# Kernel optimization log

Hardware: AMD Instinct MI355X
Metric: run time of the kernel (lower is better)

Reference implementation:

```python
import jax, jax.numpy as jnp
import numpy as np

N_NODES = 100000
EPS = 1e-12  # F.normalize eps


def _sage_conv(x, src, dst, deg, Wl, bl, Wr):
    # mean aggregation of neighbor (source) features at destination nodes
    agg = jax.ops.segment_sum(x[src], dst, num_segments=N_NODES)  # [N, F]
    agg = agg / jnp.maximum(deg, 1.0)[:, None]
    out = agg @ Wl + bl + x @ Wr  # lin_l(mean(x_j)) + lin_r(x_i)
    # normalize=True -> L2 row normalization
    norm = jnp.sqrt(jnp.sum(out * out, axis=-1, keepdims=True))
    return out / jnp.maximum(norm, EPS)


def setup_inputs() -> dict:
    key = jax.random.key(0)
    ks = jax.random.split(key, 10)
    F_IN, H, C = 14, 32, 2
    x = jax.random.normal(ks[0], (N_NODES, F_IN), dtype=jnp.float32)
    edge_index = jax.random.randint(ks[1], (2, 6400000), 0, N_NODES, dtype=jnp.int32)
    def glorot(k, shape):
        lim = float(np.sqrt(6.0 / (shape[0] + shape[1])))
        return jax.random.uniform(k, shape, jnp.float32, -lim, lim)
    return {
        "x": x,
        "edge_index": edge_index,
        "W1l": glorot(ks[2], (F_IN, H)), "b1": jnp.zeros((H,), jnp.float32),
        "W1r": glorot(ks[3], (F_IN, H)),
        "W2l": glorot(ks[4], (H, H)), "b2": jnp.zeros((H,), jnp.float32),
        "W2r": glorot(ks[5], (H, H)),
        "Wlin": glorot(ks[6], (H, C)), "blin": jnp.zeros((C,), jnp.float32),
    }


def reference(x, edge_index, W1l, b1, W1r, W2l, b2, W2r, Wlin, blin):
    src, dst = edge_index[0], edge_index[1]
    deg = jax.ops.segment_sum(jnp.ones_like(dst, dtype=x.dtype), dst,
                              num_segments=N_NODES)  # in-degree per node
    h = jax.nn.relu(_sage_conv(x, src, dst, deg, W1l, b1, W1r))
    # dropout p=0.2 is identity at inference
    h = jax.nn.relu(_sage_conv(h, src, dst, deg, W2l, b2, W2r))
    return h @ Wlin + blin  # [N, num_classes]
```

## Files before the change

### kernel.cpp

```cpp
#include <hip/hip_runtime.h>
#include <hip/hip_bf16.h>


#define CHA 16384
#define MAXBH 800
#define CAPH 9728
#define NPB 128

static __device__ __forceinline__ unsigned short f2bf(float f) {
    unsigned u = __float_as_uint(f);
    unsigned r = (u + 0x7FFFu + ((u >> 16) & 1u)) >> 16;
    return (unsigned short)r;
}
#define BF_LO(u) __uint_as_float((u) << 16)
#define BF_HI(u) __uint_as_float((u) & 0xFFFF0000u)

__global__ void cvt_x_bf16(const float* __restrict__ x, unsigned short* __restrict__ xb,
                           int* __restrict__ bcursor, int N, int NBH) {
    int idx = blockIdx.x * blockDim.x + threadIdx.x;
    if (idx < NBH) bcursor[idx] = idx * CAPH;
    if (idx >= N * 16) return;
    int n = idx >> 4, f = idx & 15;
    float v = (f < 14) ? x[n * 14 + f] : 0.f;
    xb[idx] = f2bf(v);
}

__global__ __launch_bounds__(1024) void partitionA(
        const int* __restrict__ src, const int* __restrict__ dst,
        int* __restrict__ bcursor, unsigned* __restrict__ part, int E, int NBH) {
    __shared__ unsigned pk[CHA];
    __shared__ int h[MAXBH], lofs[MAXBH], delta[MAXBH];
    int t = threadIdx.x;
    int base = blockIdx.x * CHA;
    int end = base + CHA; if (end > E) end = E;
    int cnt = end - base;

    int ed[16], es[16], er[16];
    for (int i = t; i < NBH; i += 1024) h[i] = 0;
    __syncthreads();
    #pragma unroll
    for (int i = 0; i < 4; ++i) {
        int j = i * 4096 + t * 4;
        if (j + 4 <= cnt) {
            int4 d4 = *(const int4*)(dst + base + j);
            int4 s4 = *(const int4*)(src + base + j);
            ed[i*4+0] = d4.x; ed[i*4+1] = d4.y; ed[i*4+2] = d4.z; ed[i*4+3] = d4.w;
            es[i*4+0] = s4.x; es[i*4+1] = s4.y; es[i*4+2] = s4.z; es[i*4+3] = s4.w;
            er[i*4+0] = atomicAdd(&h[d4.x >> 7], 1);
            er[i*4+1] = atomicAdd(&h[d4.y >> 7], 1);
            er[i*4+2] = atomicAdd(&h[d4.z >> 7], 1);
            er[i*4+3] = atomicAdd(&h[d4.w >> 7], 1);
        } else {
            #pragma unroll
            for (int k = 0; k < 4; ++k) {
                if (j + k < cnt) {
                    ed[i*4+k] = dst[base + j + k];
                    es[i*4+k] = src[base + j + k];
                    er[i*4+k] = atomicAdd(&h[ed[i*4+k] >> 7], 1);
                } else ed[i*4+k] = -1;
            }
        }
    }
    __syncthreads();
    if (t < 64) {
        int vals[13];
        int run = 0;
        int b13 = t * 13;
        #pragma unroll
        for (int i = 0; i < 13; ++i) {
            int idx = b13 + i;
            int x = (idx < NBH) ? h[idx] : 0;
            run += x;
            vals[i] = run;
        }
        int tot = run, sc = run;
        #pragma unroll
        for (int off = 1; off < 64; off <<= 1) {
            int nv = __shfl_up(sc, off);
            if (t >= off) sc += nv;
        }
        int excl = sc - tot;
        #pragma unroll
        for (int i = 0; i < 13; ++i) {
            int idx = b13 + i;
            if (idx < NBH) {
                h[idx] = excl + vals[i];
                lofs[idx] = excl + (i ? vals[i - 1] : 0);
            }
        }
    }
    __syncthreads();
    if (t < NBH) {
        int excl = lofs[t];
        int v = h[t] - excl;
        int g = v ? atomicAdd(&bcursor[t], v) : 0;
        delta[t] = g - excl;
    }
    __syncthreads();
    #pragma unroll
    for (int i = 0; i < 16; ++i) {
        int d = ed[i];
        if (d >= 0) {
            int b = d >> 7;
            pk[lofs[b] + er[i]] = ((unsigned)(d & 127) << 24) | (unsigned)es[i];
        }
    }
    __syncthreads();
    int wid = t >> 6, lane = t & 63;
    for (int b = wid; b < NBH; b += 16) {
        int s = lofs[b];
        int e2 = h[b];
        int dlt = delta[b];
        int lim = (b + 1) * CAPH;
        for (int k = s + lane; k < e2; k += 64) {
            int gidx = dlt + k;
            if (gidx < lim) part[gidx] = pk[k];
        }
    }
}

__global__ __launch_bounds__(1024) void partitionB_sort(
        const unsigned* __restrict__ part, const int* __restrict__ bcursor,
        int* __restrict__ deg, int* __restrict__ offs, int* __restrict__ nlo,
        int* __restrict__ sorted_src, int N, int HALF) {
    __shared__ int pk2[CAPH];
    __shared__ int hh[256], keyofs[256];
    __shared__ int sTot;
    int hbid = blockIdx.x;
    int t = threadIdx.x;
    int start = hbid * CAPH;
    int end = bcursor[hbid];
    if (end > start + CAPH) end = start + CAPH;
    unsigned ce[10];
    int rk[10];
    if (t < 256) hh[t] = 0;
    __syncthreads();
    #pragma unroll
    for (int i = 0; i < 10; ++i) {
        int idx = start + t + i * 1024;
        unsigned p = 0xFFFFFFFFu;
        int r = 0;
        if (idx < end) {
            p = part[idx];
            int key = (int)(p >> 24) * 2 + (((int)(p & 0xFFFFFFu) < HALF) ? 0 : 1);
            r = atomicAdd(&hh[key], 1);
        }
        ce[i] = p;
        rk[i] = r;
    }
    __syncthreads();
    if (t < 64) {
        int b4 = t * 4;
        int v0 = hh[b4], v1 = hh[b4 + 1], v2 = hh[b4 + 2], v3 = hh[b4 + 3];
        int s1 = v0 + v1, s2 = s1 + v2, s3 = s2 + v3;
        int sc = s3;
        #pragma unroll
        for (int off = 1; off < 64; off <<= 1) {
            int nv = __shfl_up(sc, off);
            if (t >= off) sc += nv;
        }
        int excl = sc - s3;
        keyofs[b4]     = excl;
        keyofs[b4 + 1] = excl + v0;
        keyofs[b4 + 2] = excl + s1;
        keyofs[b4 + 3] = excl + s2;
        if (t == 63) sTot = excl + s3;
    }
    __syncthreads();
    if (t < 128) {
        int lo = hh[2 * t];
        int d = lo + hh[2 * t + 1];
        int excl = keyofs[2 * t];
        int node = hbid * 128 + t;
        if (node < N) {
            deg[node] = d;
            offs[node] = start + excl;
            nlo[node] = lo;
        }
    }
    #pragma unroll
    for (int i = 0; i < 10; ++i) {
        unsigned p = ce[i];
        if (p != 0xFFFFFFFFu) {
            int s = (int)(p & 0xFFFFFFu);
            int key = (int)(p >> 24) * 2 + ((s < HALF) ? 0 : 1);
            int pos = keyofs[key] + rk[i];
            if (pos < CAPH) pk2[pos] = s;
        }
    }
    __syncthreads();
    int tot = sTot; if (tot > CAPH) tot = CAPH;
    for (int i = t; i < tot; i += 1024)
        sorted_src[start + i] = pk2[i];
}

__global__ __launch_bounds__(256) void gather14_dense1(
        const uint4* __restrict__ xb4, const float* __restrict__ x,
        const int* __restrict__ sorted_src, const int* __restrict__ offs,
        const int* __restrict__ deg,
        const float* __restrict__ W1l, const float* __restrict__ b1,
        const float* __restrict__ W1r,
        float* __restrict__ hbuf, unsigned short* __restrict__ hb, int N) {
    __shared__ float swl[448], swr[448], sb1[32];
    int t = threadIdx.x;
    for (int i = t; i < 448; i += 256) { swl[i] = W1l[i]; swr[i] = W1r[i]; }
    if (t < 32) sb1[t] = b1[t];
    __syncthreads();

    int node = blockIdx.x * 32 + (t >> 3);
    int sub = t & 7, ep = sub >> 1, half = sub & 1;
    int lanebase = (t & 63) & ~7;
    bool valid = node < N;
    int js = valid ? offs[node] : 0;
    int d  = valid ? deg[node] : 0;
    int je = js + d;
    float x0 = 0.f, x1 = 0.f;
    if (valid && sub < 7) {
        x0 = x[node * 14 + sub * 2];
        x1 = x[node * 14 + sub * 2 + 1];
    }

    float a[8] = {0,0,0,0,0,0,0,0};
    int j = js + ep;
    for (; j + 12 < je; j += 16) {
        int s0 = sorted_src[j], s1 = sorted_src[j + 4];
        int s2 = sorted_src[j + 8], s3 = sorted_src[j + 12];
        uint4 u0 = xb4[s0 * 2 + half], u1 = xb4[s1 * 2 + half];
        uint4 u2 = xb4[s2 * 2 + half], u3 = xb4[s3 * 2 + half];
        a[0] += (BF_LO(u0.x) + BF_LO(u1.x)) + (BF_LO(u2.x) + BF_LO(u3.x));
        a[1] += (BF_HI(u0.x) + BF_HI(u1.x)) + (BF_HI(u2.x) + BF_HI(u3.x));
        a[2] += (BF_LO(u0.y) + BF_LO(u1.y)) + (BF_LO(u2.y) + BF_LO(u3.y));
        a[3] += (BF_HI(u0.y) + BF_HI(u1.y)) + (BF_HI(u2.y) + BF_HI(u3.y));
        a[4] += (BF_LO(u0.z) + BF_LO(u1.z)) + (BF_LO(u2.z) + BF_LO(u3.z));
        a[5] += (BF_HI(u0.z) + BF_HI(u1.z)) + (BF_HI(u2.z) + BF_HI(u3.z));
        a[6] += (BF_LO(u0.w) + BF_LO(u1.w)) + (BF_LO(u2.w) + BF_LO(u3.w));
        a[7] += (BF_HI(u0.w) + BF_HI(u1.w)) + (BF_HI(u2.w) + BF_HI(u3.w));
    }
    for (; j + 4 < je; j += 8) {
        int s0 = sorted_src[j], s1 = sorted_src[j + 4];
        uint4 u0 = xb4[s0 * 2 + half], u1 = xb4[s1 * 2 + half];
        a[0] += BF_LO(u0.x) + BF_LO(u1.x);
        a[1] += BF_HI(u0.x) + BF_HI(u1.x);
        a[2] += BF_LO(u0.y) + BF_LO(u1.y);
        a[3] += BF_HI(u0.y) + BF_HI(u1.y);
        a[4] += BF_LO(u0.z) + BF_LO(u1.z);
        a[5] += BF_HI(u0.z) + BF_HI(u1.z);
        a[6] += BF_LO(u0.w) + BF_LO(u1.w);
        a[7] += BF_HI(u0.w) + BF_HI(u1.w);
    }
    for (; j < je; j += 4) {
        uint4 u0 = xb4[sorted_src[j] * 2 + half];
        a[0] += BF_LO(u0.x); a[1] += BF_HI(u0.x);
        a[2] += BF_LO(u0.y); a[3] += BF_HI(u0.y);
        a[4] += BF_LO(u0.z); a[5] += BF_HI(u0.z);
        a[6] += BF_LO(u0.w); a[7] += BF_HI(u0.w);
    }
    #pragma unroll
    for (int i = 0; i < 8; ++i) {
        a[i] += __shfl_xor(a[i], 2);
        a[i] += __shfl_xor(a[i], 4);
    }

    float inv = 1.0f / ((d > 0) ? (float)d : 1.0f);
    float acc[4];
    #pragma unroll
    for (int i = 0; i < 4; ++i) acc[i] = sb1[sub * 4 + i];
    #pragma unroll
    for (int k = 0; k < 14; ++k) {
        float ag = __shfl(a[k & 7], lanebase + (k >> 3)) * inv;
        float xv = __shfl((k & 1) ? x1 : x0, lanebase + (k >> 1));
        float4 wl = *(const float4*)&swl[k * 32 + sub * 4];
        float4 wr = *(const float4*)&swr[k * 32 + sub * 4];
        acc[0] += ag * wl.x + xv * wr.x;
        acc[1] += ag * wl.y + xv * wr.y;
        acc[2] += ag * wl.z + xv * wr.z;
        acc[3] += ag * wl.w + xv * wr.w;
    }
    float ss = 0.f;
    #pragma unroll
    for (int i = 0; i < 4; ++i) ss += acc[i] * acc[i];
    ss += __shfl_xor(ss, 1); ss += __shfl_xor(ss, 2); ss += __shfl_xor(ss, 4);
    float invn = 1.f / fmaxf(sqrtf(ss), 1e-12f);
    if (valid) {
        float hv[4];
        #pragma unroll
        for (int i = 0; i < 4; ++i) hv[i] = fmaxf(acc[i] * invn, 0.f);
        *(float4*)(hbuf + (size_t)node * 32 + sub * 4) =
            make_float4(hv[0], hv[1], hv[2], hv[3]);
        uint2 pb;
        pb.x = (unsigned)f2bf(hv[0]) | ((unsigned)f2bf(hv[1]) << 16);
        pb.y = (unsigned)f2bf(hv[2]) | ((unsigned)f2bf(hv[3]) << 16);
        *(uint2*)(hb + (size_t)node * 32 + sub * 4) = pb;
    }
}

__global__ __launch_bounds__(256) void gather32_p0(
        const uint4* __restrict__ hb, const int* __restrict__ sorted_src,
        const int* __restrict__ offs, const int* __restrict__ nlo,
        float4* __restrict__ agg2a, int N) {
    int idx = blockIdx.x * blockDim.x + threadIdx.x;
    int n = idx >> 2;
    if (n >= N) return;
    int q = idx & 3;
    int start = offs[n];
    int jend = nlo[n];
    float a0=0,a1=0,a2=0,a3=0,a4=0,a5=0,a6=0,a7=0;
    int j = 0;
    for (; j + 8 <= jend; j += 8) {
        int s0 = sorted_src[start + j + 0];
        int s1 = sorted_src[start + j + 1];
        int s2 = sorted_src[start + j + 2];
        int s3 = sorted_src[start + j + 3];
        int s4 = sorted_src[start + j + 4];
        int s5 = sorted_src[start + j + 5];
        int s6 = sorted_src[start + j + 6];
        int s7 = sorted_src[start + j + 7];
        uint4 u0 = hb[s0 * 4 + q];
        uint4 u1 = hb[s1 * 4 + q];
        uint4 u2 = hb[s2 * 4 + q];
        uint4 u3 = hb[s3 * 4 + q];
        uint4 u4 = hb[s4 * 4 + q];
        uint4 u5 = hb[s5 * 4 + q];
        uint4 u6 = hb[s6 * 4 + q];
        uint4 u7 = hb[s7 * 4 + q];
        a0 += (BF_LO(u0.x)+BF_LO(u1.x)+BF_LO(u2.x)+BF_LO(u3.x))
            + (BF_LO(u4.x)+BF_LO(u5.x)+BF_LO(u6.x)+BF_LO(u7.x));
        a1 += (BF_HI(u0.x)+BF_HI(u1.x)+BF_HI(u2.x)+BF_HI(u3.x))
            + (BF_HI(u4.x)+BF_HI(u5.x)+BF_HI(u6.x)+BF_HI(u7.x));
        a2 += (BF_LO(u0.y)+BF_LO(u1.y)+BF_LO(u2.y)+BF_LO(u3.y))
            + (BF_LO(u4.y)+BF_LO(u5.y)+BF_LO(u6.y)+BF_LO(u7.y));
        a3 += (BF_HI(u0.y)+BF_HI(u1.y)+BF_HI(u2.y)+BF_HI(u3.y))
            + (BF_HI(u4.y)+BF_HI(u5.y)+BF_HI(u6.y)+BF_HI(u7.y));
        a4 += (BF_LO(u0.z)+BF_LO(u1.z)+BF_LO(u2.z)+BF_LO(u3.z))
            + (BF_LO(u4.z)+BF_LO(u5.z)+BF_LO(u6.z)+BF_LO(u7.z));
        a5 += (BF_HI(u0.z)+BF_HI(u1.z)+BF_HI(u2.z)+BF_HI(u3.z))
            + (BF_HI(u4.z)+BF_HI(u5.z)+BF_HI(u6.z)+BF_HI(u7.z));
        a6 += (BF_LO(u0.w)+BF_LO(u1.w)+BF_LO(u2.w)+BF_LO(u3.w))
            + (BF_LO(u4.w)+BF_LO(u5.w)+BF_LO(u6.w)+BF_LO(u7.w));
        a7 += (BF_HI(u0.w)+BF_HI(u1.w)+BF_HI(u2.w)+BF_HI(u3.w))
            + (BF_HI(u4.w)+BF_HI(u5.w)+BF_HI(u6.w)+BF_HI(u7.w));
    }
    for (; j + 4 <= jend; j += 4) {
        int s0 = sorted_src[start + j + 0];
        int s1 = sorted_src[start + j + 1];
        int s2 = sorted_src[start + j + 2];
        int s3 = sorted_src[start + j + 3];
        uint4 u0 = hb[s0 * 4 + q];
        uint4 u1 = hb[s1 * 4 + q];
        uint4 u2 = hb[s2 * 4 + q];
        uint4 u3 = hb[s3 * 4 + q];
        a0 += BF_LO(u0.x)+BF_LO(u1.x)+BF_LO(u2.x)+BF_LO(u3.x);
        a1 += BF_HI(u0.x)+BF_HI(u1.x)+BF_HI(u2.x)+BF_HI(u3.x);
        a2 += BF_LO(u0.y)+BF_LO(u1.y)+BF_LO(u2.y)+BF_LO(u3.y);
        a3 += BF_HI(u0.y)+BF_HI(u1.y)+BF_HI(u2.y)+BF_HI(u3.y);
        a4 += BF_LO(u0.z)+BF_LO(u1.z)+BF_LO(u2.z)+BF_LO(u3.z);
        a5 += BF_HI(u0.z)+BF_HI(u1.z)+BF_HI(u2.z)+BF_HI(u3.z);
        a6 += BF_LO(u0.w)+BF_LO(u1.w)+BF_LO(u2.w)+BF_LO(u3.w);
        a7 += BF_HI(u0.w)+BF_HI(u1.w)+BF_HI(u2.w)+BF_HI(u3.w);
    }
    for (; j < jend; ++j) {
        uint4 u0 = hb[sorted_src[start + j] * 4 + q];
        a0 += BF_LO(u0.x); a1 += BF_HI(u0.x);
        a2 += BF_LO(u0.y); a3 += BF_HI(u0.y);
        a4 += BF_LO(u0.z); a5 += BF_HI(u0.z);
        a6 += BF_LO(u0.w); a7 += BF_HI(u0.w);
    }
    agg2a[n * 8 + q * 2 + 0] = make_float4(a0, a1, a2, a3);
    agg2a[n * 8 + q * 2 + 1] = make_float4(a4, a5, a6, a7);
}

__global__ __launch_bounds__(256) void gather32_p1(
        const uint4* __restrict__ hb, const int* __restrict__ sorted_src,
        const int* __restrict__ offs, const int* __restrict__ deg,
        const int* __restrict__ nlo, float4* __restrict__ agg2b, int N) {
    int idx = blockIdx.x * blockDim.x + threadIdx.x;
    int n = idx >> 2;
    if (n >= N) return;
    int q = idx & 3;
    int start = offs[n];
    int d = deg[n];
    int j = nlo[n];
    float a0=0,a1=0,a2=0,a3=0,a4=0,a5=0,a6=0,a7=0;
    for (; j + 8 <= d; j += 8) {
        int s0 = sorted_src[start + j + 0];
        int s1 = sorted_src[start + j + 1];
        int s2 = sorted_src[start + j + 2];
        int s3 = sorted_src[start + j + 3];
        int s4 = sorted_src[start + j + 4];
        int s5 = sorted_src[start + j + 5];
        int s6 = sorted_src[start + j + 6];
        int s7 = sorted_src[start + j + 7];
        uint4 u0 = hb[s0 * 4 + q];
        uint4 u1 = hb[s1 * 4 + q];
        uint4 u2 = hb[s2 * 4 + q];
        uint4 u3 = hb[s3 * 4 + q];
        uint4 u4 = hb[s4 * 4 + q];
        uint4 u5 = hb[s5 * 4 + q];
        uint4 u6 = hb[s6 * 4 + q];
        uint4 u7 = hb[s7 * 4 + q];
        a0 += (BF_LO(u0.x)+BF_LO(u1.x)+BF_LO(u2.x)+BF_LO(u3.x))
            + (BF_LO(u4.x)+BF_LO(u5.x)+BF_LO(u6.x)+BF_LO(u7.x));
        a1 += (BF_HI(u0.x)+BF_HI(u1.x)+BF_HI(u2.x)+BF_HI(u3.x))
            + (BF_HI(u4.x)+BF_HI(u5.x)+BF_HI(u6.x)+BF_HI(u7.x));
        a2 += (BF_LO(u0.y)+BF_LO(u1.y)+BF_LO(u2.y)+BF_LO(u3.y))
            + (BF_LO(u4.y)+BF_LO(u5.y)+BF_LO(u6.y)+BF_LO(u7.y));
        a3 += (BF_HI(u0.y)+BF_HI(u1.y)+BF_HI(u2.y)+BF_HI(u3.y))
            + (BF_HI(u4.y)+BF_HI(u5.y)+BF_HI(u6.y)+BF_HI(u7.y));
        a4 += (BF_LO(u0.z)+BF_LO(u1.z)+BF_LO(u2.z)+BF_LO(u3.z))
            + (BF_LO(u4.z)+BF_LO(u5.z)+BF_LO(u6.z)+BF_LO(u7.z));
        a5 += (BF_HI(u0.z)+BF_HI(u1.z)+BF_HI(u2.z)+BF_HI(u3.z))
            + (BF_HI(u4.z)+BF_HI(u5.z)+BF_HI(u6.z)+BF_HI(u7.z));
        a6 += (BF_LO(u0.w)+BF_LO(u1.w)+BF_LO(u2.w)+BF_LO(u3.w))
            + (BF_LO(u4.w)+BF_LO(u5.w)+BF_LO(u6.w)+BF_LO(u7.w));
        a7 += (BF_HI(u0.w)+BF_HI(u1.w)+BF_HI(u2.w)+BF_HI(u3.w))
            + (BF_HI(u4.w)+BF_HI(u5.w)+BF_HI(u6.w)+BF_HI(u7.w));
    }
    for (; j + 4 <= d; j += 4) {
        int s0 = sorted_src[start + j + 0];
        int s1 = sorted_src[start + j + 1];
        int s2 = sorted_src[start + j + 2];
        int s3 = sorted_src[start + j + 3];
        uint4 u0 = hb[s0 * 4 + q];
        uint4 u1 = hb[s1 * 4 + q];
        uint4 u2 = hb[s2 * 4 + q];
        uint4 u3 = hb[s3 * 4 + q];
        a0 += BF_LO(u0.x)+BF_LO(u1.x)+BF_LO(u2.x)+BF_LO(u3.x);
        a1 += BF_HI(u0.x)+BF_HI(u1.x)+BF_HI(u2.x)+BF_HI(u3.x);
        a2 += BF_LO(u0.y)+BF_LO(u1.y)+BF_LO(u2.y)+BF_LO(u3.y);
        a3 += BF_HI(u0.y)+BF_HI(u1.y)+BF_HI(u2.y)+BF_HI(u3.y);
        a4 += BF_LO(u0.z)+BF_LO(u1.z)+BF_LO(u2.z)+BF_LO(u3.z);
        a5 += BF_HI(u0.z)+BF_HI(u1.z)+BF_HI(u2.z)+BF_HI(u3.z);
        a6 += BF_LO(u0.w)+BF_LO(u1.w)+BF_LO(u2.w)+BF_LO(u3.w);
        a7 += BF_HI(u0.w)+BF_HI(u1.w)+BF_HI(u2.w)+BF_HI(u3.w);
    }
    for (; j < d; ++j) {
        uint4 u0 = hb[sorted_src[start + j] * 4 + q];
        a0 += BF_LO(u0.x); a1 += BF_HI(u0.x);
        a2 += BF_LO(u0.y); a3 += BF_HI(u0.y);
        a4 += BF_LO(u0.z); a5 += BF_HI(u0.z);
        a6 += BF_LO(u0.w); a7 += BF_HI(u0.w);
    }
    agg2b[n * 8 + q * 2 + 0] = make_float4(a0, a1, a2, a3);
    agg2b[n * 8 + q * 2 + 1] = make_float4(a4, a5, a6, a7);
}

__global__ __launch_bounds__(256) void dense2(
        const float* __restrict__ h, const float* __restrict__ agg2a,
        const float* __restrict__ agg2b, const int* __restrict__ deg,
        const float* __restrict__ W2l, const float* __restrict__ b2,
        const float* __restrict__ W2r, const float* __restrict__ Wlin,
        const float* __restrict__ blin, float* __restrict__ out, int N) {
    __shared__ float sa[NPB * 33];
    __shared__ float sh2[NPB * 33];
    __shared__ float swl[32 * 32], swr[32 * 32], swo[64], sb[32], sbo[2];
    int t = threadIdx.x;
    int nb = blockIdx.x * NPB;
    int nn = N - nb; if (nn > NPB) nn = NPB;
    const float4* ga = (const float4*)(agg2a + (size_t)nb * 32);
    const float4* gb = (const float4*)(agg2b + (size_t)nb * 32);
    const float4* gh = (const float4*)(h + (size_t)nb * 32);
    for (int i = t; i < nn * 8; i += 256) {
        int row = i >> 3;
        int dv = deg[nb + row];
        float inv = 1.0f / ((dv > 0) ? (float)dv : 1.0f);
        float4 va = ga[i], vb = gb[i];
        float* d = &sa[row * 33 + (i & 7) * 4];
        d[0] = (va.x + vb.x) * inv; d[1] = (va.y + vb.y) * inv;
        d[2] = (va.z + vb.z) * inv; d[3] = (va.w + vb.w) * inv;
        float4 w = gh[i];
        float* e = &sh2[row * 33 + (i & 7) * 4];
        e[0] = w.x; e[1] = w.y; e[2] = w.z; e[3] = w.w;
    }
    for (int i = t; i < 1024; i += 256) { swl[i] = W2l[i]; swr[i] = W2r[i]; }
    if (t < 64) swo[t] = Wlin[t];
    if (t < 32) sb[t] = b2[t];
    if (t < 2) sbo[t] = blin[t];
    __syncthreads();
    int q2 = t & 3;
    int p = t >> 2;
    int l0 = p * 2, l1 = l0 + 1;
    float acc0[8], acc1[8];
    #pragma unroll
    for (int j = 0; j < 8; ++j) { acc0[j] = sb[q2 * 8 + j]; acc1[j] = acc0[j]; }
    for (int k = 0; k < 32; ++k) {
        float a0 = sa[l0 * 33 + k],  a1 = sa[l1 * 33 + k];
        float h0 = sh2[l0 * 33 + k], h1 = sh2[l1 * 33 + k];
        const float4* wl4 = (const float4*)&swl[k * 32 + q2 * 8];
        const float4* wr4 = (const float4*)&swr[k * 32 + q2 * 8];
        float4 wla = wl4[0], wlb = wl4[1], wra = wr4[0], wrb = wr4[1];
        acc0[0] += a0 * wla.x + h0 * wra.x;  acc1[0] += a1 * wla.x + h1 * wra.x;
        acc0[1] += a0 * wla.y + h0 * wra.y;  acc1[1] += a1 * wla.y + h1 * wra.y;
        acc0[2] += a0 * wla.z + h0 * wra.z;  acc1[2] += a1 * wla.z + h1 * wra.z;
        acc0[3] += a0 * wla.w + h0 * wra.w;  acc1[3] += a1 * wla.w + h1 * wra.w;
        acc0[4] += a0 * wlb.x + h0 * wrb.x;  acc1[4] += a1 * wlb.x + h1 * wrb.x;
        acc0[5] += a0 * wlb.y + h0 * wrb.y;  acc1[5] += a1 * wlb.y + h1 * wrb.y;
        acc0[6] += a0 * wlb.z + h0 * wrb.z;  acc1[6] += a1 * wlb.z + h1 * wrb.z;
        acc0[7] += a0 * wlb.w + h0 * wrb.w;  acc1[7] += a1 * wlb.w + h1 * wrb.w;
    }
    float ss0 = 0.f, ss1 = 0.f;
    #pragma unroll
    for (int j = 0; j < 8; ++j) { ss0 += acc0[j] * acc0[j]; ss1 += acc1[j] * acc1[j]; }
    ss0 += __shfl_xor(ss0, 1); ss0 += __shfl_xor(ss0, 2);
    ss1 += __shfl_xor(ss1, 1); ss1 += __shfl_xor(ss1, 2);
    float inv0 = 1.f / fmaxf(sqrtf(ss0), 1e-12f);
    float inv1 = 1.f / fmaxf(sqrtf(ss1), 1e-12f);
    float o00 = 0.f, o01 = 0.f, o10 = 0.f, o11 = 0.f;
    #pragma unroll
    for (int j = 0; j < 8; ++j) {
        float hv0 = fmaxf(acc0[j] * inv0, 0.f);
        float hv1 = fmaxf(acc1[j] * inv1, 0.f);
        int kk = q2 * 8 + j;
        o00 += hv0 * swo[kk * 2 + 0];
        o01 += hv0 * swo[kk * 2 + 1];
        o10 += hv1 * swo[kk * 2 + 0];
        o11 += hv1 * swo[kk * 2 + 1];
    }
    o00 += __shfl_xor(o00, 1); o00 += __shfl_xor(o00, 2);
    o01 += __shfl_xor(o01, 1); o01 += __shfl_xor(o01, 2);
    o10 += __shfl_xor(o10, 1); o10 += __shfl_xor(o10, 2);
    o11 += __shfl_xor(o11, 1); o11 += __shfl_xor(o11, 2);
    if (q2 == 0) {
        int n0 = nb + l0, n1 = nb + l1;
        if (n0 < N) { out[n0 * 2 + 0] = o00 + sbo[0]; out[n0 * 2 + 1] = o01 + sbo[1]; }
        if (n1 < N) { out[n1 * 2 + 0] = o10 + sbo[0]; out[n1 * 2 + 1] = o11 + sbo[1]; }
    }
}

extern "C" void kernel_launch(void* const* d_in, const int* in_sizes, int n_in,
                              void* d_out, int out_size, void* d_ws, size_t ws_size,
                              hipStream_t stream) {
    const float* x    = (const float*)d_in[0];
    const int*   ei   = (const int*)d_in[1];
    const float* W1l  = (const float*)d_in[2];
    const float* b1   = (const float*)d_in[3];
    const float* W1r  = (const float*)d_in[4];
    const float* W2l  = (const float*)d_in[5];
    const float* b2   = (const float*)d_in[6];
    const float* W2r  = (const float*)d_in[7];
    const float* Wlin = (const float*)d_in[8];
    const float* blin = (const float*)d_in[9];
    float* out = (float*)d_out;

    const int N = in_sizes[0] / 14;
    const int E = in_sizes[1] / 2;
    const int* src = ei;
    const int* dst = ei + E;
    const int NBH = (N + 127) / 128;
    const int HALF = N / 2;

    char* ws = (char*)d_ws;
    size_t off = 0;
    auto alloc = [&](size_t bytes) -> void* {
        void* p = ws + off;
        off = (off + bytes + 255) & ~(size_t)255;
        return p;
    };
    int*            bcursor    = (int*)alloc((size_t)NBH * 4);
    unsigned*       part       = (unsigned*)alloc((size_t)NBH * CAPH * 4);
    int*            sorted_src = (int*)alloc((size_t)NBH * CAPH * 4);
    int*            deg        = (int*)alloc((size_t)N * 4);
    int*            offs       = (int*)alloc((size_t)N * 4);
    int*            nlo        = (int*)alloc((size_t)N * 4);
    unsigned short* xb         = (unsigned short*)alloc((size_t)N * 16 * 2);
    float*          hbuf       = (float*)alloc((size_t)N * 32 * 4);
    unsigned short* hb         = (unsigned short*)alloc((size_t)N * 32 * 2);
    float*          agg2b      = (float*)alloc((size_t)N * 32 * 4);
    float*          agg2a      = (float*)part;
    (void)ws_size; (void)n_in; (void)out_size;

    const int NB32 = (N + 31) / 32;

    cvt_x_bf16<<<(N * 16 + 255) / 256, 256, 0, stream>>>(x, xb, bcursor, N, NBH);
    partitionA<<<(E + CHA - 1) / CHA, 1024, 0, stream>>>(src, dst, bcursor, part, E, NBH);
    partitionB_sort<<<NBH, 1024, 0, stream>>>(
        part, bcursor, deg, offs, nlo, sorted_src, N, HALF);
    gather14_dense1<<<NB32, 256, 0, stream>>>(
        (const uint4*)xb, x, sorted_src, offs, deg, W1l, b1, W1r, hbuf, hb, N);
    gather32_p0<<<(N * 4 + 255) / 256, 256, 0, stream>>>(
        (const uint4*)hb, sorted_src, offs, nlo, (float4*)agg2a, N);
    gather32_p1<<<(N * 4 + 255) / 256, 256, 0, stream>>>(
        (const uint4*)hb, sorted_src, offs, deg, nlo, (float4*)agg2b, N);
    dense2<<<(N + NPB - 1) / NPB, 256, 0, stream>>>(
        hbuf, agg2a, agg2b, deg, W2l, b2, W2r, Wlin, blin, out, N);
}
```

Measured before the change: 276.3 us.

## Fuse second gather half with dense2 and fold bf16 conversion into partitioning

The bf16 conversion of x moves into partitionA as a grid-stride loop, and bcursor is zeroed with a memset. partitionA drops its shared-memory staging and block-wide scan and scatters straight to global using per-block atomic bases, with half the chunk size and thread count. The second half of the layer-2 gather is fused with the dense2 epilogue, so the agg2b buffer and one launch go away. The risks are less coalesced scatter writes in partitionA and the gather now competing with the shared-memory weight load for occupancy.

```diff
diff --git a/kernel.cpp b/kernel.cpp
--- a/kernel.cpp
+++ b/kernel.cpp
@@ -2,10 +2,9 @@
 #include <hip/hip_bf16.h>
 
 
-#define CHA 16384
+#define CHA 8192
 #define MAXBH 800
 #define CAPH 9728
-#define NPB 128
 
 static __device__ __forceinline__ unsigned short f2bf(float f) {
     unsigned u = __float_as_uint(f);
@@ -15,32 +14,29 @@
 #define BF_LO(u) __uint_as_float((u) << 16)
 #define BF_HI(u) __uint_as_float((u) & 0xFFFF0000u)
 
-__global__ void cvt_x_bf16(const float* __restrict__ x, unsigned short* __restrict__ xb,
-                           int* __restrict__ bcursor, int N, int NBH) {
-    int idx = blockIdx.x * blockDim.x + threadIdx.x;
-    if (idx < NBH) bcursor[idx] = idx * CAPH;
-    if (idx >= N * 16) return;
-    int n = idx >> 4, f = idx & 15;
-    float v = (f < 14) ? x[n * 14 + f] : 0.f;
-    xb[idx] = f2bf(v);
-}
-
-__global__ __launch_bounds__(1024) void partitionA(
+__global__ __launch_bounds__(512) void partitionA(
+        const float* __restrict__ x, unsigned short* __restrict__ xb,
         const int* __restrict__ src, const int* __restrict__ dst,
-        int* __restrict__ bcursor, unsigned* __restrict__ part, int E, int NBH) {
-    __shared__ unsigned pk[CHA];
-    __shared__ int h[MAXBH], lofs[MAXBH], delta[MAXBH];
+        int* __restrict__ bcursor, unsigned* __restrict__ part,
+        int E, int N, int NBH) {
+    __shared__ int h[MAXBH], gb[MAXBH];
     int t = threadIdx.x;
     int base = blockIdx.x * CHA;
     int end = base + CHA; if (end > E) end = E;
     int cnt = end - base;
 
+    for (int i = blockIdx.x * 512 + t; i < N * 16; i += gridDim.x * 512) {
+        int n = i >> 4, f = i & 15;
+        float v = (f < 14) ? x[n * 14 + f] : 0.f;
+        xb[i] = f2bf(v);
+    }
+
     int ed[16], es[16], er[16];
-    for (int i = t; i < NBH; i += 1024) h[i] = 0;
+    for (int i = t; i < NBH; i += 512) h[i] = 0;
     __syncthreads();
     #pragma unroll
     for (int i = 0; i < 4; ++i) {
-        int j = i * 4096 + t * 4;
+        int j = i * 2048 + t * 4;
         if (j + 4 <= cnt) {
             int4 d4 = *(const int4*)(dst + base + j);
             int4 s4 = *(const int4*)(src + base + j);
@@ -62,59 +58,20 @@
         }
     }
     __syncthreads();
-    if (t < 64) {
-        int vals[13];
-        int run = 0;
-        int b13 = t * 13;
-        #pragma unroll
-        for (int i = 0; i < 13; ++i) {
-            int idx = b13 + i;
-            int x = (idx < NBH) ? h[idx] : 0;
-            run += x;
-            vals[i] = run;
-        }
-        int tot = run, sc = run;
-        #pragma unroll
-        for (int off = 1; off < 64; off <<= 1) {
-            int nv = __shfl_up(sc, off);
-            if (t >= off) sc += nv;
-        }
-        int excl = sc - tot;
-        #pragma unroll
-        for (int i = 0; i < 13; ++i) {
-            int idx = b13 + i;
-            if (idx < NBH) {
-                h[idx] = excl + vals[i];
-                lofs[idx] = excl + (i ? vals[i - 1] : 0);
-            }
-        }
-    }
-    __syncthreads();
-    if (t < NBH) {
-        int excl = lofs[t];
-        int v = h[t] - excl;
-        int g = v ? atomicAdd(&bcursor[t], v) : 0;
-        delta[t] = g - excl;
+    for (int i = t; i < NBH; i += 512) {
+        int v = h[i];
+        gb[i] = v ? atomicAdd(&bcursor[i], v) : 0;
     }
     __syncthreads();
     #pragma unroll
     for (int i = 0; i < 16; ++i) {
-        int d = ed[i];
-        if (d >= 0) {
-            int b = d >> 7;
-            pk[lofs[b] + er[i]] = ((unsigned)(d & 127) << 24) | (unsigned)es[i];
-        }
-    }
-    __syncthreads();
-    int wid = t >> 6, lane = t & 63;
-    for (int b = wid; b < NBH; b += 16) {
-        int s = lofs[b];
-        int e2 = h[b];
-        int dlt = delta[b];
-        int lim = (b + 1) * CAPH;
-        for (int k = s + lane; k < e2; k += 64) {
-            int gidx = dlt + k;
-            if (gidx < lim) part[gidx] = pk[k];
+        int dd = ed[i];
+        if (dd >= 0) {
+            int b = dd >> 7;
+            int pos = gb[b] + er[i];
+            if (pos < CAPH)
+                part[(size_t)b * CAPH + pos] =
+                    ((unsigned)(dd & 127) << 24) | (unsigned)es[i];
         }
     }
 }
@@ -129,8 +86,9 @@
     int hbid = blockIdx.x;
     int t = threadIdx.x;
     int start = hbid * CAPH;
-    int end = bcursor[hbid];
-    if (end > start + CAPH) end = start + CAPH;
+    int cc = bcursor[hbid];
+    if (cc > CAPH) cc = CAPH;
+    int end = start + cc;
     unsigned ce[10];
     int rk[10];
     if (t < 256) hh[t] = 0;
@@ -369,17 +327,29 @@
     agg2a[n * 8 + q * 2 + 1] = make_float4(a4, a5, a6, a7);
 }
 
-__global__ __launch_bounds__(256) void gather32_p1(
+__global__ __launch_bounds__(256) void gather32p1_dense2(
         const uint4* __restrict__ hb, const int* __restrict__ sorted_src,
         const int* __restrict__ offs, const int* __restrict__ deg,
-        const int* __restrict__ nlo, float4* __restrict__ agg2b, int N) {
-    int idx = blockIdx.x * blockDim.x + threadIdx.x;
-    int n = idx >> 2;
-    if (n >= N) return;
-    int q = idx & 3;
-    int start = offs[n];
-    int d = deg[n];
-    int j = nlo[n];
+        const int* __restrict__ nlo, const float* __restrict__ agg2a,
+        const float* __restrict__ hbuf,
+        const float* __restrict__ W2l, const float* __restrict__ b2,
+        const float* __restrict__ W2r, const float* __restrict__ Wlin,
+        const float* __restrict__ blin, float* __restrict__ out, int N) {
+    __shared__ float sa[64 * 33];
+    __shared__ float sh2[64 * 33];
+    __shared__ float swl[1024], swr[1024], swo[64], sb[32], sbo[2];
+    int t = threadIdx.x;
+    for (int i = t; i < 1024; i += 256) { swl[i] = W2l[i]; swr[i] = W2r[i]; }
+    if (t < 64) swo[t] = Wlin[t];
+    if (t < 32) sb[t] = b2[t];
+    if (t < 2) sbo[t] = blin[t];
+
+    int row = t >> 2, q = t & 3;
+    int n = blockIdx.x * 64 + row;
+    bool valid = n < N;
+    int start = valid ? offs[n] : 0;
+    int d = valid ? deg[n] : 0;
+    int j = valid ? nlo[n] : 0;
     float a0=0,a1=0,a2=0,a3=0,a4=0,a5=0,a6=0,a7=0;
     for (; j + 8 <= d; j += 8) {
         int s0 = sorted_src[start + j + 0];
@@ -440,89 +410,59 @@
         a4 += BF_LO(u0.z); a5 += BF_HI(u0.z);
         a6 += BF_LO(u0.w); a7 += BF_HI(u0.w);
     }
-    agg2b[n * 8 + q * 2 + 0] = make_float4(a0, a1, a2, a3);
-    agg2b[n * 8 + q * 2 + 1] = make_float4(a4, a5, a6, a7);
-}
-
-__global__ __launch_bounds__(256) void dense2(
-        const float* __restrict__ h, const float* __restrict__ agg2a,
-        const float* __restrict__ agg2b, const int* __restrict__ deg,
-        const float* __restrict__ W2l, const float* __restrict__ b2,
-        const float* __restrict__ W2r, const float* __restrict__ Wlin,
-        const float* __restrict__ blin, float* __restrict__ out, int N) {
-    __shared__ float sa[NPB * 33];
-    __shared__ float sh2[NPB * 33];
-    __shared__ float swl[32 * 32], swr[32 * 32], swo[64], sb[32], sbo[2];
-    int t = threadIdx.x;
-    int nb = blockIdx.x * NPB;
-    int nn = N - nb; if (nn > NPB) nn = NPB;
-    const float4* ga = (const float4*)(agg2a + (size_t)nb * 32);
-    const float4* gb = (const float4*)(agg2b + (size_t)nb * 32);
-    const float4* gh = (const float4*)(h + (size_t)nb * 32);
-    for (int i = t; i < nn * 8; i += 256) {
-        int row = i >> 3;
-        int dv = deg[nb + row];
-        float inv = 1.0f / ((dv > 0) ? (float)dv : 1.0f);
-        float4 va = ga[i], vb = gb[i];
-        float* d = &sa[row * 33 + (i & 7) * 4];
-        d[0] = (va.x + vb.x) * inv; d[1] = (va.y + vb.y) * inv;
-        d[2] = (va.z + vb.z) * inv; d[3] = (va.w + vb.w) * inv;
-        float4 w = gh[i];
-        float* e = &sh2[row * 33 + (i & 7) * 4];
-        e[0] = w.x; e[1] = w.y; e[2] = w.z; e[3] = w.w;
-    }
-    for (int i = t; i < 1024; i += 256) { swl[i] = W2l[i]; swr[i] = W2r[i]; }
-    if (t < 64) swo[t] = Wlin[t];
-    if (t < 32) sb[t] = b2[t];
-    if (t < 2) sbo[t] = blin[t];
-    __syncthreads();
-    int q2 = t & 3;
-    int p = t >> 2;
-    int l0 = p * 2, l1 = l0 + 1;
-    float acc0[8], acc1[8];
-    #pragma unroll
-    for (int j = 0; j < 8; ++j) { acc0[j] = sb[q2 * 8 + j]; acc1[j] = acc0[j]; }
+    if (valid) {
+        float inv = 1.0f / ((d > 0) ? (float)d : 1.0f);
+        const float4* ga = (const float4*)(agg2a + (size_t)n * 32 + q * 8);
+        float4 v0 = ga[0], v1 = ga[1];
+        float* sd = &sa[row * 33 + q * 8];
+        sd[0] = (v0.x + a0) * inv; sd[1] = (v0.y + a1) * inv;
+        sd[2] = (v0.z + a2) * inv; sd[3] = (v0.w + a3) * inv;
+        sd[4] = (v1.x + a4) * inv; sd[5] = (v1.y + a5) * inv;
+        sd[6] = (v1.z + a6) * inv; sd[7] = (v1.w + a7) * inv;
+        const float4* gh = (const float4*)(hbuf + (size_t)n * 32 + q * 8);
+        float4 h0 = gh[0], h1 = gh[1];
+        float* se = &sh2[row * 33 + q * 8];
+        se[0] = h0.x; se[1] = h0.y; se[2] = h0.z; se[3] = h0.w;
+        se[4] = h1.x; se[5] = h1.y; se[6] = h1.z; se[7] = h1.w;
+    }
+    __syncthreads();
+
+    float acc[8];
+    #pragma unroll
+    for (int i = 0; i < 8; ++i) acc[i] = sb[q * 8 + i];
     for (int k = 0; k < 32; ++k) {
-        float a0 = sa[l0 * 33 + k],  a1 = sa[l1 * 33 + k];
-        float h0 = sh2[l0 * 33 + k], h1 = sh2[l1 * 33 + k];
-        const float4* wl4 = (const float4*)&swl[k * 32 + q2 * 8];
-        const float4* wr4 = (const float4*)&swr[k * 32 + q2 * 8];
+        float av = sa[row * 33 + k];
+        float hv = sh2[row * 33 + k];
+        const float4* wl4 = (const float4*)&swl[k * 32 + q * 8];
+        const float4* wr4 = (const float4*)&swr[k * 32 + q * 8];
         float4 wla = wl4[0], wlb = wl4[1], wra = wr4[0], wrb = wr4[1];
-        acc0[0] += a0 * wla.x + h0 * wra.x;  acc1[0] += a1 * wla.x + h1 * wra.x;
-        acc0[1] += a0 * wla.y + h0 * wra.y;  acc1[1] += a1 * wla.y + h1 * wra.y;
-        acc0[2] += a0 * wla.z + h0 * wra.z;  acc1[2] += a1 * wla.z + h1 * wra.z;
-        acc0[3] += a0 * wla.w + h0 * wra.w;  acc1[3] += a1 * wla.w + h1 * wra.w;
-        acc0[4] += a0 * wlb.x + h0 * wrb.x;  acc1[4] += a1 * wlb.x + h1 * wrb.x;
-        acc0[5] += a0 * wlb.y + h0 * wrb.y;  acc1[5] += a1 * wlb.y + h1 * wrb.y;
-        acc0[6] += a0 * wlb.z + h0 * wrb.z;  acc1[6] += a1 * wlb.z + h1 * wrb.z;
-        acc0[7] += a0 * wlb.w + h0 * wrb.w;  acc1[7] += a1 * wlb.w + h1 * wrb.w;
-    }
-    float ss0 = 0.f, ss1 = 0.f;
-    #pragma unroll
-    for (int j = 0; j < 8; ++j) { ss0 += acc0[j] * acc0[j]; ss1 += acc1[j] * acc1[j]; }
-    ss0 += __shfl_xor(ss0, 1); ss0 += __shfl_xor(ss0, 2);
-    ss1 += __shfl_xor(ss1, 1); ss1 += __shfl_xor(ss1, 2);
-    float inv0 = 1.f / fmaxf(sqrtf(ss0), 1e-12f);
-    float inv1 = 1.f / fmaxf(sqrtf(ss1), 1e-12f);
-    float o00 = 0.f, o01 = 0.f, o10 = 0.f, o11 = 0.f;
-    #pragma unroll
-    for (int j = 0; j < 8; ++j) {
-        float hv0 = fmaxf(acc0[j] * inv0, 0.f);
-        float hv1 = fmaxf(acc1[j] * inv1, 0.f);
-        int kk = q2 * 8 + j;
-        o00 += hv0 * swo[kk * 2 + 0];
-        o01 += hv0 * swo[kk * 2 + 1];
-        o10 += hv1 * swo[kk * 2 + 0];
-        o11 += hv1 * swo[kk * 2 + 1];
-    }
-    o00 += __shfl_xor(o00, 1); o00 += __shfl_xor(o00, 2);
-    o01 += __shfl_xor(o01, 1); o01 += __shfl_xor(o01, 2);
-    o10 += __shfl_xor(o10, 1); o10 += __shfl_xor(o10, 2);
-    o11 += __shfl_xor(o11, 1); o11 += __shfl_xor(o11, 2);
-    if (q2 == 0) {
-        int n0 = nb + l0, n1 = nb + l1;
-        if (n0 < N) { out[n0 * 2 + 0] = o00 + sbo[0]; out[n0 * 2 + 1] = o01 + sbo[1]; }
-        if (n1 < N) { out[n1 * 2 + 0] = o10 + sbo[0]; out[n1 * 2 + 1] = o11 + sbo[1]; }
+        acc[0] += av * wla.x + hv * wra.x;
+        acc[1] += av * wla.y + hv * wra.y;
+        acc[2] += av * wla.z + hv * wra.z;
+        acc[3] += av * wla.w + hv * wra.w;
+        acc[4] += av * wlb.x + hv * wrb.x;
+        acc[5] += av * wlb.y + hv * wrb.y;
+        acc[6] += av * wlb.z + hv * wrb.z;
+        acc[7] += av * wlb.w + hv * wrb.w;
+    }
+    float ss = 0.f;
+    #pragma unroll
+    for (int i = 0; i < 8; ++i) ss += acc[i] * acc[i];
+    ss += __shfl_xor(ss, 1); ss += __shfl_xor(ss, 2);
+    float invn = 1.f / fmaxf(sqrtf(ss), 1e-12f);
+    float o0 = 0.f, o1 = 0.f;
+    #pragma unroll
+    for (int i = 0; i < 8; ++i) {
+        float hv = fmaxf(acc[i] * invn, 0.f);
+        int kk = q * 8 + i;
+        o0 += hv * swo[kk * 2 + 0];
+        o1 += hv * swo[kk * 2 + 1];
+    }
+    o0 += __shfl_xor(o0, 1); o0 += __shfl_xor(o0, 2);
+    o1 += __shfl_xor(o1, 1); o1 += __shfl_xor(o1, 2);
+    if (q == 0 && valid) {
+        out[n * 2 + 0] = o0 + sbo[0];
+        out[n * 2 + 1] = o1 + sbo[1];
     }
 }
 
@@ -564,22 +504,19 @@
     unsigned short* xb         = (unsigned short*)alloc((size_t)N * 16 * 2);
     float*          hbuf       = (float*)alloc((size_t)N * 32 * 4);
     unsigned short* hb         = (unsigned short*)alloc((size_t)N * 32 * 2);
-    float*          agg2b      = (float*)alloc((size_t)N * 32 * 4);
     float*          agg2a      = (float*)part;
     (void)ws_size; (void)n_in; (void)out_size;
 
-    const int NB32 = (N + 31) / 32;
-
-    cvt_x_bf16<<<(N * 16 + 255) / 256, 256, 0, stream>>>(x, xb, bcursor, N, NBH);
-    partitionA<<<(E + CHA - 1) / CHA, 1024, 0, stream>>>(src, dst, bcursor, part, E, NBH);
+    hipMemsetAsync(bcursor, 0, (size_t)NBH * 4, stream);
+    partitionA<<<(E + CHA - 1) / CHA, 512, 0, stream>>>(
+        x, xb, src, dst, bcursor, part, E, N, NBH);
     partitionB_sort<<<NBH, 1024, 0, stream>>>(
         part, bcursor, deg, offs, nlo, sorted_src, N, HALF);
-    gather14_dense1<<<NB32, 256, 0, stream>>>(
+    gather14_dense1<<<(N + 31) / 32, 256, 0, stream>>>(
         (const uint4*)xb, x, sorted_src, offs, deg, W1l, b1, W1r, hbuf, hb, N);
     gather32_p0<<<(N * 4 + 255) / 256, 256, 0, stream>>>(
         (const uint4*)hb, sorted_src, offs, nlo, (float4*)agg2a, N);
-    gather32_p1<<<(N * 4 + 255) / 256, 256, 0, stream>>>(
-        (const uint4*)hb, sorted_src, offs, deg, nlo, (float4*)agg2b, N);
-    dense2<<<(N + NPB - 1) / NPB, 256, 0, stream>>>(
-        hbuf, agg2a, agg2b, deg, W2l, b2, W2r, Wlin, blin, out, N);
-}
+    gather32p1_dense2<<<(N + 63) / 64, 256, 0, stream>>>(
+        (const uint4*)hb, sorted_src, offs, deg, nlo, agg2a, hbuf,
+        W2l, b2, W2r, Wlin, blin, out, N);
+}
```

Result: slower. 309.6 us (+12.0%).
